# Kernel tuning notes

Hardware: AMD Instinct MI355X
Metric: run time of the kernel (lower is better)

## Reference

```python
import jax, jax.numpy as jnp
import numpy as np

COMMITMENT_COST = 0.25
EPSILON = 1e-05


def setup_inputs() -> dict:
    key = jax.random.key(0)
    k1, k2, k3 = jax.random.split(key, 3)
    inputs = jax.random.normal(k1, (32, 256, 32, 32), dtype=jnp.float32)
    embedding = jax.random.normal(k2, (256, 1024), dtype=jnp.float32)
    cluster_size = jax.random.uniform(k3, (1024,), dtype=jnp.float32)
    return {"inputs": inputs, "embedding": embedding, "cluster_size": cluster_size}


def reference(inputs, embedding, cluster_size):
    B = inputs.shape[0]
    D, K = embedding.shape  # (embedding_dim, num_embeddings)

    # Faithful to source: reshape (B,C,H,W) -> (-1, D) WITHOUT permuting.
    flat_input = inputs.reshape(-1, D)  # (N, D), N = B*H*W (since C == D)

    distances = (
        jnp.sum(flat_input ** 2, axis=1, keepdims=True)
        + jnp.sum(embedding ** 2, axis=0, keepdims=True)
        - 2.0 * flat_input @ embedding
    )  # (N, K)
    encoding_indices = jnp.argmin(distances, axis=1)  # (N,)

    # Gather codes: embedding[:, idx].T -> (N, D), reshape back to input shape
    quantized = jnp.take(embedding, encoding_indices, axis=1).T.reshape(inputs.shape)

    e_latent_loss = jnp.mean((jax.lax.stop_gradient(quantized) - inputs) ** 2)
    q_latent_loss = jnp.mean((quantized - jax.lax.stop_gradient(inputs)) ** 2)
    commitment_loss = COMMITMENT_COST * q_latent_loss
    vq_loss = e_latent_loss + commitment_loss

    # Straight-through estimator
    quantized_ste = inputs + jax.lax.stop_gradient(quantized - inputs)

    avg_probs = cluster_size / (jnp.sum(cluster_size) + EPSILON)
    perplexity = jnp.exp(-jnp.sum(avg_probs * jnp.log(avg_probs + EPSILON)))
    used_codes = jnp.sum((cluster_size > EPSILON).astype(jnp.float32))
    code_usage_rate = used_codes / K

    return (quantized_ste, vq_loss, perplexity, code_usage_rate,
            encoding_indices.reshape(B, -1))
```

## Files before the change

kernel.cpp:

```cpp
#include <hip/hip_runtime.h>


constexpr int DIM = 256;
constexpr int NK  = 1024;
constexpr int RR  = 16;

__global__ __launch_bounds__(256) void enorm_kernel(
    const float* __restrict__ emb, float* __restrict__ enorm) {
  int k = blockIdx.x * 256 + threadIdx.x;
  float s = 0.f;
  for (int d = 0; d < DIM; ++d) {
    float e = emb[(size_t)d * NK + k];
    s = fmaf(e, e, s);
  }
  enorm[k] = s;
}

__global__ __launch_bounds__(256) void argmin_kernel(
    const float* __restrict__ x, const float* __restrict__ emb,
    const float* __restrict__ enorm, int* __restrict__ idx_out,
    float* __restrict__ idx_out_f) {
  __shared__ float4 xs[RR * DIM / 4];
  __shared__ float red_v[4][RR];
  __shared__ int   red_i[4][RR];

  const int tid = threadIdx.x;
  const size_t base = (size_t)blockIdx.x * (RR * DIM);

  {
    const float4* src = (const float4*)(x + base);
    #pragma unroll
    for (int i = 0; i < 4; ++i) xs[tid + 256 * i] = src[tid + 256 * i];
  }
  __syncthreads();

  float acc[RR][4];
  #pragma unroll
  for (int r = 0; r < RR; ++r) {
    #pragma unroll
    for (int j = 0; j < 4; ++j) acc[r][j] = 0.f;
  }

  const int k0 = tid * 4;
  for (int d4 = 0; d4 < DIM / 4; ++d4) {
    const float4 e0 = *(const float4*)(emb + (size_t)(d4 * 4 + 0) * NK + k0);
    const float4 e1 = *(const float4*)(emb + (size_t)(d4 * 4 + 1) * NK + k0);
    const float4 e2 = *(const float4*)(emb + (size_t)(d4 * 4 + 2) * NK + k0);
    const float4 e3 = *(const float4*)(emb + (size_t)(d4 * 4 + 3) * NK + k0);
    #pragma unroll
    for (int r = 0; r < RR; ++r) {
      const float4 xv = xs[r * (DIM / 4) + d4];
      acc[r][0] = fmaf(xv.x, e0.x, fmaf(xv.y, e1.x, fmaf(xv.z, e2.x, fmaf(xv.w, e3.x, acc[r][0]))));
      acc[r][1] = fmaf(xv.x, e0.y, fmaf(xv.y, e1.y, fmaf(xv.z, e2.y, fmaf(xv.w, e3.y, acc[r][1]))));
      acc[r][2] = fmaf(xv.x, e0.z, fmaf(xv.y, e1.z, fmaf(xv.z, e2.z, fmaf(xv.w, e3.z, acc[r][2]))));
      acc[r][3] = fmaf(xv.x, e0.w, fmaf(xv.y, e1.w, fmaf(xv.z, e2.w, fmaf(xv.w, e3.w, acc[r][3]))));
    }
  }

  const float4 en = *(const float4*)(enorm + k0);
  const int lane = tid & 63;
  const int wv   = tid >> 6;

  for (int r = 0; r < RR; ++r) {
    float bv = en.x - 2.f * acc[r][0];
    int   bi = k0;
    { float v = en.y - 2.f * acc[r][1]; if (v < bv) { bv = v; bi = k0 + 1; } }
    { float v = en.z - 2.f * acc[r][2]; if (v < bv) { bv = v; bi = k0 + 2; } }
    { float v = en.w - 2.f * acc[r][3]; if (v < bv) { bv = v; bi = k0 + 3; } }
    for (int off = 32; off > 0; off >>= 1) {
      float ov = __shfl_xor(bv, off);
      int   oi = __shfl_xor(bi, off);
      if (ov < bv || (ov == bv && oi < bi)) { bv = ov; bi = oi; }
    }
    if (lane == 0) { red_v[wv][r] = bv; red_i[wv][r] = bi; }
  }
  __syncthreads();

  if (tid < RR) {
    float bv = red_v[0][tid];
    int   bi = red_i[0][tid];
    #pragma unroll
    for (int w = 1; w < 4; ++w) {
      float v = red_v[w][tid]; int i2 = red_i[w][tid];
      if (v < bv || (v == bv && i2 < bi)) { bv = v; bi = i2; }
    }
    const int n = blockIdx.x * RR + tid;
    idx_out[n]   = bi;
    idx_out_f[n] = (float)bi;
  }
}

__global__ __launch_bounds__(256) void gather_loss_kernel(
    const float* __restrict__ x, const float* __restrict__ emb,
    const int* __restrict__ idx, float* __restrict__ out_q,
    float* __restrict__ partial) {
  const int tid = threadIdx.x;
  const size_t base = (size_t)blockIdx.x * 2048;
  float local = 0.f;
  #pragma unroll
  for (int h = 0; h < 2; ++h) {
    const size_t g = base + (size_t)h * 1024 + (size_t)tid * 4;
    const int n = (int)(g >> 8);
    const int d = (int)(g & 255);
    const int k = idx[n];
    const float* ep = emb + (size_t)d * NK + k;
    float4 q;
    q.x = ep[0]; q.y = ep[NK]; q.z = ep[2 * NK]; q.w = ep[3 * NK];
    const float4 xv = *(const float4*)(x + g);
    *(float4*)(out_q + g) = q;
    const float dx = q.x - xv.x, dy = q.y - xv.y, dz = q.z - xv.z, dw = q.w - xv.w;
    local = fmaf(dx, dx, local);
    local = fmaf(dy, dy, local);
    local = fmaf(dz, dz, local);
    local = fmaf(dw, dw, local);
  }
  for (int off = 32; off > 0; off >>= 1) local += __shfl_down(local, off);
  __shared__ float wsum[4];
  if ((tid & 63) == 0) wsum[tid >> 6] = local;
  __syncthreads();
  if (tid == 0) partial[blockIdx.x] = (wsum[0] + wsum[1]) + (wsum[2] + wsum[3]);
}

__global__ __launch_bounds__(1024) void finalize_kernel(
    const float* __restrict__ partial, int np,
    const float* __restrict__ cs, float* __restrict__ out_s,
    float inv_count) {
  __shared__ float sd[1024];
  const int tid = threadIdx.x;

  float s = 0.f;
  for (int i = tid; i < np; i += 1024) s += partial[i];
  sd[tid] = s; __syncthreads();
  for (int st = 512; st > 0; st >>= 1) {
    if (tid < st) sd[tid] += sd[tid + st];
    __syncthreads();
  }
  const float total_sq = sd[0];
  __syncthreads();

  const float c = cs[tid];
  sd[tid] = c; __syncthreads();
  for (int st = 512; st > 0; st >>= 1) {
    if (tid < st) sd[tid] += sd[tid + st];
    __syncthreads();
  }
  const float S = sd[0];
  __syncthreads();

  const float p = c / (S + 1e-5f);
  sd[tid] = p * logf(p + 1e-5f);
  __syncthreads();
  for (int st = 512; st > 0; st >>= 1) {
    if (tid < st) sd[tid] += sd[tid + st];
    __syncthreads();
  }
  const float T = sd[0];
  __syncthreads();

  sd[tid] = (c > 1e-5f) ? 1.f : 0.f;
  __syncthreads();
  for (int st = 512; st > 0; st >>= 1) {
    if (tid < st) sd[tid] += sd[tid + st];
    __syncthreads();
  }
  const float U = sd[0];

  if (tid == 0) {
    out_s[0] = 1.25f * total_sq * inv_count;
    out_s[1] = expf(-T);
    out_s[2] = U * (1.f / 1024.f);
  }
}

extern "C" void kernel_launch(void* const* d_in, const int* in_sizes, int n_in,
                              void* d_out, int out_size, void* d_ws, size_t ws_size,
                              hipStream_t stream) {
  const float* x   = (const float*)d_in[0];
  const float* emb = (const float*)d_in[1];
  const float* cs  = (const float*)d_in[2];
  float* out = (float*)d_out;

  const int N = in_sizes[0] / DIM;
  const size_t ND = (size_t)N * DIM;

  float* enorm   = (float*)d_ws;
  int*   idxw    = (int*)((char*)d_ws + NK * sizeof(float));
  float* partial = (float*)((char*)d_ws + NK * sizeof(float) + (size_t)N * sizeof(int));

  const int nGather = (int)(ND / 2048);

  enorm_kernel<<<NK / 256, 256, 0, stream>>>(emb, enorm);
  argmin_kernel<<<N / RR, 256, 0, stream>>>(x, emb, enorm, idxw, out + ND + 3);
  gather_loss_kernel<<<nGather, 256, 0, stream>>>(x, emb, idxw, out, partial);
  finalize_kernel<<<1, 1024, 0, stream>>>(partial, nGather, cs, out + ND,
                                          1.0f / (float)ND);
}
```

Measured before the change: 302.3 us.

## Double-buffer embedding loads in argmin loop and fold factor two into norms

Software-pipelines the argmin inner loop so the embedding float4 loads for the next d4 step are issued while the FMAs of the current step run, using two register sets. It also stores half the squared code norms so the comparison needs no multiply by two, and adds a launch-bounds occupancy hint of four blocks per CU. The extra prefetch registers plus 64 accumulators may raise register pressure or cause spills under the occupancy constraint.

Result: slower. 1.165 ms (+285.5%).

```diff
diff --git a/kernel.cpp b/kernel.cpp
--- a/kernel.cpp
+++ b/kernel.cpp
@@ -13,10 +13,26 @@
     float e = emb[(size_t)d * NK + k];
     s = fmaf(e, e, s);
   }
-  enorm[k] = s;
-}
-
-__global__ __launch_bounds__(256) void argmin_kernel(
+  enorm[k] = 0.5f * s;
+}
+
+#define LOADE(E0, E1, E2, E3, D4)                                           \
+  E0 = *(const float4*)(emb + (size_t)((D4) * 4 + 0) * NK + k0);            \
+  E1 = *(const float4*)(emb + (size_t)((D4) * 4 + 1) * NK + k0);            \
+  E2 = *(const float4*)(emb + (size_t)((D4) * 4 + 2) * NK + k0);            \
+  E3 = *(const float4*)(emb + (size_t)((D4) * 4 + 3) * NK + k0);
+
+#define COMP(E0, E1, E2, E3, D4)                                                                 \
+  _Pragma("unroll")                                                                              \
+  for (int r = 0; r < RR; ++r) {                                                                 \
+    const float4 xv = xs[r * (DIM / 4) + (D4)];                                                  \
+    acc[r][0] = fmaf(xv.x, E0.x, fmaf(xv.y, E1.x, fmaf(xv.z, E2.x, fmaf(xv.w, E3.x, acc[r][0])))); \
+    acc[r][1] = fmaf(xv.x, E0.y, fmaf(xv.y, E1.y, fmaf(xv.z, E2.y, fmaf(xv.w, E3.y, acc[r][1])))); \
+    acc[r][2] = fmaf(xv.x, E0.z, fmaf(xv.y, E1.z, fmaf(xv.z, E2.z, fmaf(xv.w, E3.z, acc[r][2])))); \
+    acc[r][3] = fmaf(xv.x, E0.w, fmaf(xv.y, E1.w, fmaf(xv.z, E2.w, fmaf(xv.w, E3.w, acc[r][3])))); \
+  }
+
+__global__ __launch_bounds__(256, 4) void argmin_kernel(
     const float* __restrict__ x, const float* __restrict__ emb,
     const float* __restrict__ enorm, int* __restrict__ idx_out,
     float* __restrict__ idx_out_f) {
@@ -42,31 +58,29 @@
   }
 
   const int k0 = tid * 4;
-  for (int d4 = 0; d4 < DIM / 4; ++d4) {
-    const float4 e0 = *(const float4*)(emb + (size_t)(d4 * 4 + 0) * NK + k0);
-    const float4 e1 = *(const float4*)(emb + (size_t)(d4 * 4 + 1) * NK + k0);
-    const float4 e2 = *(const float4*)(emb + (size_t)(d4 * 4 + 2) * NK + k0);
-    const float4 e3 = *(const float4*)(emb + (size_t)(d4 * 4 + 3) * NK + k0);
-    #pragma unroll
-    for (int r = 0; r < RR; ++r) {
-      const float4 xv = xs[r * (DIM / 4) + d4];
-      acc[r][0] = fmaf(xv.x, e0.x, fmaf(xv.y, e1.x, fmaf(xv.z, e2.x, fmaf(xv.w, e3.x, acc[r][0]))));
-      acc[r][1] = fmaf(xv.x, e0.y, fmaf(xv.y, e1.y, fmaf(xv.z, e2.y, fmaf(xv.w, e3.y, acc[r][1]))));
-      acc[r][2] = fmaf(xv.x, e0.z, fmaf(xv.y, e1.z, fmaf(xv.z, e2.z, fmaf(xv.w, e3.z, acc[r][2]))));
-      acc[r][3] = fmaf(xv.x, e0.w, fmaf(xv.y, e1.w, fmaf(xv.z, e2.w, fmaf(xv.w, e3.w, acc[r][3]))));
-    }
-  }
+  float4 a0, a1, a2, a3, b0, b1, b2, b3;
+
+  LOADE(a0, a1, a2, a3, 0)
+  for (int d4 = 0; d4 < (DIM / 4) - 2; d4 += 2) {
+    LOADE(b0, b1, b2, b3, d4 + 1)
+    COMP(a0, a1, a2, a3, d4)
+    LOADE(a0, a1, a2, a3, d4 + 2)
+    COMP(b0, b1, b2, b3, d4 + 1)
+  }
+  LOADE(b0, b1, b2, b3, (DIM / 4) - 1)
+  COMP(a0, a1, a2, a3, (DIM / 4) - 2)
+  COMP(b0, b1, b2, b3, (DIM / 4) - 1)
 
   const float4 en = *(const float4*)(enorm + k0);
   const int lane = tid & 63;
   const int wv   = tid >> 6;
 
   for (int r = 0; r < RR; ++r) {
-    float bv = en.x - 2.f * acc[r][0];
+    float bv = en.x - acc[r][0];
     int   bi = k0;
-    { float v = en.y - 2.f * acc[r][1]; if (v < bv) { bv = v; bi = k0 + 1; } }
-    { float v = en.z - 2.f * acc[r][2]; if (v < bv) { bv = v; bi = k0 + 2; } }
-    { float v = en.w - 2.f * acc[r][3]; if (v < bv) { bv = v; bi = k0 + 3; } }
+    { float v = en.y - acc[r][1]; if (v < bv) { bv = v; bi = k0 + 1; } }
+    { float v = en.z - acc[r][2]; if (v < bv) { bv = v; bi = k0 + 2; } }
+    { float v = en.w - acc[r][3]; if (v < bv) { bv = v; bi = k0 + 3; } }
     for (int off = 32; off > 0; off >>= 1) {
       float ov = __shfl_xor(bv, off);
       int   oi = __shfl_xor(bi, off);
```

## Double-buffer embedding tiles into LDS via async global_load_lds in argmin

Applied to the files above, without the earlier changes.

The argmin kernel now stages the input rows and each 4-row slice of the embedding into shared memory using direct global-to-LDS loads. The embedding slices are double-buffered and prefetched one step ahead, with explicit vmcnt waits. The goal is to hide global load latency behind the FMA loop. It also pre-halves the embedding norms so the per-candidate multiply by 2 is dropped, and adds an occupancy hint of 3 blocks per SM. LDS use rises to about 48KB per block, which may limit occupancy. The pipeline relies on hand-placed waitcnts with no barrier between buffer swaps, which is risky, although each thread only reads the slot it wrote itself.

After: 290.5 us. 3.9% less time.

```diff
diff --git a/kernel.cpp b/kernel.cpp
--- a/kernel.cpp
+++ b/kernel.cpp
@@ -4,6 +4,12 @@
 constexpr int DIM = 256;
 constexpr int NK  = 1024;
 constexpr int RR  = 16;
+constexpr int NG  = DIM / 4;
+
+#define GLL16(GSRC, LDST)                                                      \
+  __builtin_amdgcn_global_load_lds(                                            \
+      (const __attribute__((address_space(1))) void*)(GSRC),                   \
+      (__attribute__((address_space(3))) void*)(LDST), 16, 0, 0)
 
 __global__ __launch_bounds__(256) void enorm_kernel(
     const float* __restrict__ emb, float* __restrict__ enorm) {
@@ -13,25 +19,28 @@
     float e = emb[(size_t)d * NK + k];
     s = fmaf(e, e, s);
   }
-  enorm[k] = s;
-}
-
-__global__ __launch_bounds__(256) void argmin_kernel(
+  enorm[k] = 0.5f * s;
+}
+
+__global__ __launch_bounds__(256, 3) void argmin_kernel(
     const float* __restrict__ x, const float* __restrict__ emb,
     const float* __restrict__ enorm, int* __restrict__ idx_out,
     float* __restrict__ idx_out_f) {
-  __shared__ float4 xs[RR * DIM / 4];
+  __shared__ float xs[RR * DIM];
+  __shared__ float es[2][4][NK];
   __shared__ float red_v[4][RR];
   __shared__ int   red_i[4][RR];
 
   const int tid = threadIdx.x;
-  const size_t base = (size_t)blockIdx.x * (RR * DIM);
-
-  {
-    const float4* src = (const float4*)(x + base);
-    #pragma unroll
-    for (int i = 0; i < 4; ++i) xs[tid + 256 * i] = src[tid + 256 * i];
-  }
+  const int k0  = tid * 4;
+  const size_t xbase = (size_t)blockIdx.x * (RR * DIM);
+
+  #pragma unroll
+  for (int i = 0; i < 4; ++i)
+    GLL16(x + xbase + (size_t)(tid + 256 * i) * 4, &xs[(tid + 256 * i) * 4]);
+  #pragma unroll
+  for (int r = 0; r < 4; ++r)
+    GLL16(emb + (size_t)r * NK + k0, &es[0][r][k0]);
   __syncthreads();
 
   float acc[RR][4];
@@ -41,15 +50,27 @@
     for (int j = 0; j < 4; ++j) acc[r][j] = 0.f;
   }
 
-  const int k0 = tid * 4;
-  for (int d4 = 0; d4 < DIM / 4; ++d4) {
-    const float4 e0 = *(const float4*)(emb + (size_t)(d4 * 4 + 0) * NK + k0);
-    const float4 e1 = *(const float4*)(emb + (size_t)(d4 * 4 + 1) * NK + k0);
-    const float4 e2 = *(const float4*)(emb + (size_t)(d4 * 4 + 2) * NK + k0);
-    const float4 e3 = *(const float4*)(emb + (size_t)(d4 * 4 + 3) * NK + k0);
+  #pragma unroll 2
+  for (int g = 0; g < NG; ++g) {
+    if (g < NG - 1) {
+      const float* src = emb + (size_t)((g + 1) * 4) * NK + k0;
+      #pragma unroll
+      for (int r = 0; r < 4; ++r)
+        GLL16(src + (size_t)r * NK, &es[(g + 1) & 1][r][k0]);
+      asm volatile("s_waitcnt vmcnt(4)" ::: "memory");
+    } else {
+      asm volatile("s_waitcnt vmcnt(0)" ::: "memory");
+    }
+    __builtin_amdgcn_sched_barrier(0);
+
+    const int b = g & 1;
+    const float4 e0 = *(const float4*)&es[b][0][k0];
+    const float4 e1 = *(const float4*)&es[b][1][k0];
+    const float4 e2 = *(const float4*)&es[b][2][k0];
+    const float4 e3 = *(const float4*)&es[b][3][k0];
     #pragma unroll
     for (int r = 0; r < RR; ++r) {
-      const float4 xv = xs[r * (DIM / 4) + d4];
+      const float4 xv = *(const float4*)&xs[r * DIM + g * 4];
       acc[r][0] = fmaf(xv.x, e0.x, fmaf(xv.y, e1.x, fmaf(xv.z, e2.x, fmaf(xv.w, e3.x, acc[r][0]))));
       acc[r][1] = fmaf(xv.x, e0.y, fmaf(xv.y, e1.y, fmaf(xv.z, e2.y, fmaf(xv.w, e3.y, acc[r][1]))));
       acc[r][2] = fmaf(xv.x, e0.z, fmaf(xv.y, e1.z, fmaf(xv.z, e2.z, fmaf(xv.w, e3.z, acc[r][2]))));
@@ -62,11 +83,11 @@
   const int wv   = tid >> 6;
 
   for (int r = 0; r < RR; ++r) {
-    float bv = en.x - 2.f * acc[r][0];
+    float bv = en.x - acc[r][0];
     int   bi = k0;
-    { float v = en.y - 2.f * acc[r][1]; if (v < bv) { bv = v; bi = k0 + 1; } }
-    { float v = en.z - 2.f * acc[r][2]; if (v < bv) { bv = v; bi = k0 + 2; } }
-    { float v = en.w - 2.f * acc[r][3]; if (v < bv) { bv = v; bi = k0 + 3; } }
+    { float v = en.y - acc[r][1]; if (v < bv) { bv = v; bi = k0 + 1; } }
+    { float v = en.z - acc[r][2]; if (v < bv) { bv = v; bi = k0 + 2; } }
+    { float v = en.w - acc[r][3]; if (v < bv) { bv = v; bi = k0 + 3; } }
     for (int off = 32; off > 0; off >>= 1) {
       float ov = __shfl_xor(bv, off);
       int   oi = __shfl_xor(bi, off);
```
